# Kernel optimization log

Measured on AMD Instinct MI355X. Metric: run time of the kernel, lower is better.

The kernel has to match this reference:

```python
import jax, jax.numpy as jnp
import numpy as np

D_MODEL = 1024
NHEAD = 16
D_K = D_MODEL // NHEAD


def sparsemax(z):
    # sparsemax along last axis (Martins & Astudillo 2016)
    n = z.shape[-1]
    z_sorted = jnp.flip(jnp.sort(z, axis=-1), axis=-1)          # descending
    k = jnp.arange(1, n + 1, dtype=z.dtype)
    z_cumsum = jnp.cumsum(z_sorted, axis=-1)
    support = (1.0 + k * z_sorted) > z_cumsum                    # [..., n] bool
    k_max = jnp.sum(support, axis=-1, keepdims=True)             # [..., 1] int
    tau_sum = jnp.take_along_axis(z_cumsum, k_max - 1, axis=-1)
    tau = (tau_sum - 1.0) / k_max.astype(z.dtype)
    return jnp.maximum(z - tau, 0.0)


def setup_inputs() -> dict:
    key = jax.random.key(0)
    ks = jax.random.split(key, 12)
    B, S = 2, 2048
    s = 1.0 / np.sqrt(D_MODEL)
    inp = {
        'query': jax.random.normal(ks[0], (B, S, D_MODEL), jnp.float32),
        'key':   jax.random.normal(ks[1], (B, S, D_MODEL), jnp.float32),
        'value': jax.random.normal(ks[2], (B, S, D_MODEL), jnp.float32),
        'Wq': jax.random.uniform(ks[3], (D_MODEL, D_MODEL), jnp.float32, -s, s),
        'bq': jax.random.uniform(ks[4], (D_MODEL,), jnp.float32, -s, s),
        'Wk': jax.random.uniform(ks[5], (D_MODEL, D_MODEL), jnp.float32, -s, s),
        'bk': jax.random.uniform(ks[6], (D_MODEL,), jnp.float32, -s, s),
        'Wv': jax.random.uniform(ks[7], (D_MODEL, D_MODEL), jnp.float32, -s, s),
        'bv': jax.random.uniform(ks[8], (D_MODEL,), jnp.float32, -s, s),
        'Wfc': jax.random.uniform(ks[9], (D_MODEL, D_MODEL), jnp.float32, -s, s),
        'bfc': jax.random.uniform(ks[10], (D_MODEL,), jnp.float32, -s, s),
    }
    return inp


def reference(query, key, value, Wq, bq, Wk, bk, Wv, bv, Wfc, bfc):
    B, S, _ = query.shape
    # projections (torch Linear: x @ W.T + b)
    q = (query @ Wq.T + bq).reshape(B, S, NHEAD, D_K).transpose(0, 2, 1, 3)
    k = (key   @ Wk.T + bk).reshape(B, S, NHEAD, D_K).transpose(0, 2, 1, 3)
    v = (value @ Wv.T + bv).reshape(B, S, NHEAD, D_K).transpose(0, 2, 1, 3)
    # scaled dot-product with sparsemax
    logits = jnp.einsum('bhqd,bhkd->bhqk', q, k) / np.sqrt(D_K).astype(jnp.float32)
    attention = sparsemax(logits)                                # [B,H,S,S]
    attn_out = jnp.einsum('bhqk,bhkd->bhqd', attention, v)
    attn_out = attn_out.transpose(0, 2, 1, 3).reshape(B, S, D_MODEL)
    output = attn_out @ Wfc.T + bfc                              # dropout = identity (eval)
    return output, attention
```

## Files before the change

### kernel.cpp

```cpp
#include <hip/hip_runtime.h>
#include <hip/hip_bf16.h>
#include <cstdint>

#define S_LEN  2048
#define DMODEL 1024
#define NHEAD  16
#define M_ROWS 4096

typedef __attribute__((ext_vector_type(8))) short bf16x8;
typedef __attribute__((ext_vector_type(4))) float f32x4;

__device__ __forceinline__ unsigned short f2bf(float f) {
    __hip_bfloat16 h = __float2bfloat16(f);
    return __builtin_bit_cast(unsigned short, h);
}
__device__ __forceinline__ float bf2f(unsigned short u) {
    return __builtin_bit_cast(float, (unsigned)u << 16);
}
__device__ __forceinline__ uint4 pack8(float4 a, float4 b) {
    uint4 u;
    u.x = ((unsigned)f2bf(a.y) << 16) | f2bf(a.x);
    u.y = ((unsigned)f2bf(a.w) << 16) | f2bf(a.z);
    u.z = ((unsigned)f2bf(b.y) << 16) | f2bf(b.x);
    u.w = ((unsigned)f2bf(b.w) << 16) | f2bf(b.z);
    return u;
}

__device__ __forceinline__ float wave_sum64(float v) {
    v += __shfl_xor(v, 32, 64); v += __shfl_xor(v, 16, 64);
    v += __shfl_xor(v, 8, 64);  v += __shfl_xor(v, 4, 64);
    v += __shfl_xor(v, 2, 64);  v += __shfl_xor(v, 1, 64);
    return v;
}
__device__ __forceinline__ float wave_max64(float v) {
    v = fmaxf(v, __shfl_xor(v, 32, 64)); v = fmaxf(v, __shfl_xor(v, 16, 64));
    v = fmaxf(v, __shfl_xor(v, 8, 64));  v = fmaxf(v, __shfl_xor(v, 4, 64));
    v = fmaxf(v, __shfl_xor(v, 2, 64));  v = fmaxf(v, __shfl_xor(v, 1, 64));
    return v;
}
__device__ __forceinline__ int lanes_below(unsigned long long m) {
    return __builtin_amdgcn_mbcnt_hi((unsigned)(m >> 32),
           __builtin_amdgcn_mbcnt_lo((unsigned)m, 0));
}

__global__ __launch_bounds__(256)
void qkv_gemm(const float* __restrict__ xq, const float* __restrict__ xk,
              const float* __restrict__ xv,
              const float* __restrict__ Wq, const float* __restrict__ Wk,
              const float* __restrict__ Wv,
              const float* __restrict__ bq, const float* __restrict__ bk,
              const float* __restrict__ bv,
              unsigned short* __restrict__ Q_bf, unsigned short* __restrict__ K_bf,
              unsigned short* __restrict__ V_bf) {
    const int which = blockIdx.z;
    const float* A    = (which == 0) ? xq : (which == 1) ? xk : xv;
    const float* W    = (which == 0) ? Wq : (which == 1) ? Wk : Wv;
    const float* bias = (which == 0) ? bq : (which == 1) ? bk : bv;
    unsigned short* dst = (which == 0) ? Q_bf : (which == 1) ? K_bf : V_bf;

    const int row0 = blockIdx.x * 128;
    const int col0 = blockIdx.y * 128;

    __shared__ unsigned short SMEM[10240];
    unsigned short* As = SMEM;
    unsigned short* Bs = SMEM + 5120;

    const int t = threadIdx.x;
    const int wid = t >> 6, lane = t & 63;
    const int wm = wid >> 1, wn = wid & 1;
    const int l = lane & 15, quad = lane >> 4;

    f32x4 acc[4][4];
#pragma unroll
    for (int i = 0; i < 4; ++i)
#pragma unroll
        for (int j = 0; j < 4; ++j) {
            float b_ = bias[col0 + wn * 64 + j * 16 + l];
            acc[i][j] = (f32x4){ b_, b_, b_, b_ };
        }

    for (int k0 = 0; k0 < DMODEL; k0 += 32) {
        uint4 ar[2], br[2];
#pragma unroll
        for (int i = 0; i < 2; ++i) {
            const int c = t + i * 256, r = c >> 2, q = (c & 3) * 8;
            const float* ap = A + (size_t)(row0 + r) * DMODEL + k0 + q;
            const float* wp = W + (size_t)(col0 + r) * DMODEL + k0 + q;
            float4 a0 = *(const float4*)ap, a1 = *(const float4*)(ap + 4);
            float4 w0 = *(const float4*)wp, w1 = *(const float4*)(wp + 4);
            ar[i] = pack8(a0, a1);
            br[i] = pack8(w0, w1);
        }
        __syncthreads();
#pragma unroll
        for (int i = 0; i < 2; ++i) {
            const int c = t + i * 256, r = c >> 2, q = (c & 3) * 8;
            *(uint4*)&As[r * 40 + q] = ar[i];
            *(uint4*)&Bs[r * 40 + q] = br[i];
        }
        __syncthreads();
        bf16x8 a[4], b[4];
#pragma unroll
        for (int i = 0; i < 4; ++i)
            a[i] = *(const bf16x8*)&As[(wm * 64 + i * 16 + l) * 40 + quad * 8];
#pragma unroll
        for (int j = 0; j < 4; ++j)
            b[j] = *(const bf16x8*)&Bs[(wn * 64 + j * 16 + l) * 40 + quad * 8];
#pragma unroll
        for (int i = 0; i < 4; ++i)
#pragma unroll
            for (int j = 0; j < 4; ++j)
                acc[i][j] = __builtin_amdgcn_mfma_f32_16x16x32_bf16(a[i], b[j], acc[i][j], 0, 0, 0);
    }

    __syncthreads();
    unsigned short* Cs = SMEM;
#pragma unroll 1
    for (int jh = 0; jh < 2; ++jh) {
        if (wn == jh) {
#pragma unroll
            for (int i = 0; i < 4; ++i)
#pragma unroll
                for (int j = 0; j < 4; ++j)
#pragma unroll
                    for (int r = 0; r < 4; ++r)
                        Cs[(wm * 64 + i * 16 + quad * 4 + r) * 72 + j * 16 + l] =
                            f2bf(acc[i][j][r]);
        }
        __syncthreads();
#pragma unroll
        for (int it = 0; it < 4; ++it) {
            const int idx = t + it * 256;
            const int row = idx >> 3, c8 = (idx & 7) * 8;
            *(uint4*)(dst + (size_t)(row0 + row) * DMODEL + col0 + jh * 64 + c8) =
                *(const uint4*)&Cs[row * 72 + c8];
        }
        __syncthreads();
    }
}

__global__ __launch_bounds__(256)
void logits_gemm(const unsigned short* __restrict__ Q_bf,
                 const unsigned short* __restrict__ K_bf,
                 float* __restrict__ attn) {
    const int bh = blockIdx.z;
    const int b_ = bh >> 4, h = bh & 15;
    const unsigned short* Qh = Q_bf + ((size_t)b_ * S_LEN) * DMODEL + h * 64;
    const unsigned short* Kh = K_bf + ((size_t)b_ * S_LEN) * DMODEL + h * 64;
    const int row0 = blockIdx.x * 128;
    const int col0 = blockIdx.y * 128;

    __shared__ unsigned short As[128 * 72];
    __shared__ unsigned short Bs[128 * 72];

    const int t = threadIdx.x;
    const int wid = t >> 6, lane = t & 63;
    const int wm = wid >> 1, wn = wid & 1;
    const int l = lane & 15, quad = lane >> 4;

#pragma unroll
    for (int i = 0; i < 4; ++i) {
        const int c = t + i * 256, r = c >> 3, q = (c & 7) * 8;
        *(uint4*)&As[r * 72 + q] = *(const uint4*)(Qh + (size_t)(row0 + r) * DMODEL + q);
        *(uint4*)&Bs[r * 72 + q] = *(const uint4*)(Kh + (size_t)(col0 + r) * DMODEL + q);
    }
    __syncthreads();

    f32x4 acc[4][4] = {};
#pragma unroll
    for (int kk = 0; kk < 64; kk += 32) {
        bf16x8 a[4], b[4];
#pragma unroll
        for (int i = 0; i < 4; ++i)
            a[i] = *(const bf16x8*)&As[(wm * 64 + i * 16 + l) * 72 + kk + quad * 8];
#pragma unroll
        for (int j = 0; j < 4; ++j)
            b[j] = *(const bf16x8*)&Bs[(wn * 64 + j * 16 + l) * 72 + kk + quad * 8];
#pragma unroll
        for (int i = 0; i < 4; ++i)
#pragma unroll
            for (int j = 0; j < 4; ++j)
                acc[i][j] = __builtin_amdgcn_mfma_f32_16x16x32_bf16(a[i], b[j], acc[i][j], 0, 0, 0);
    }

    float* ap = attn + (size_t)bh * S_LEN * S_LEN;
#pragma unroll
    for (int i = 0; i < 4; ++i)
#pragma unroll
        for (int r = 0; r < 4; ++r) {
            const int m = row0 + wm * 64 + i * 16 + quad * 4 + r;
#pragma unroll
            for (int j = 0; j < 4; ++j) {
                const int n = col0 + wn * 64 + j * 16 + l;
                ap[(size_t)m * S_LEN + n] = acc[i][j][r] * 0.125f;
            }
        }
}

__global__ __launch_bounds__(256)
void smpv_kernel(float* __restrict__ attn, const unsigned short* __restrict__ V_bf,
                 unsigned short* __restrict__ AO_bf) {
    const int wave = threadIdx.x >> 6;
    const int lane = threadIdx.x & 63;
    const size_t row = (size_t)blockIdx.x * 4 + wave;
    const int bh = (int)(row >> 11), s = (int)(row & 2047);
    const int b_ = bh >> 4, h = bh & 15;
    float4* rp = (float4*)(attn + row * S_LEN);
    const unsigned short* Vh = V_bf + ((size_t)b_ * S_LEN) * DMODEL + h * 64;

    __shared__ uint2 list[4][512];

    float z[32];
#pragma unroll
    for (int r = 0; r < 8; ++r) {
        float4 v = rp[r * 64 + lane];
        z[4 * r + 0] = v.x; z[4 * r + 1] = v.y;
        z[4 * r + 2] = v.z; z[4 * r + 3] = v.w;
    }
    float m = z[0];
#pragma unroll
    for (int j = 1; j < 32; ++j) m = fmaxf(m, z[j]);
    m = wave_max64(m);

    float tau = m - 1.0f;
#pragma unroll 1
    for (int it = 0; it < 8; ++it) {
        float ss = 0.0f, kk = 0.0f;
#pragma unroll
        for (int j = 0; j < 32; ++j)
            if (z[j] > tau) { ss += z[j]; kk += 1.0f; }
        ss = wave_sum64(ss); kk = wave_sum64(kk);
        tau = (ss - 1.0f) / kk;
    }

#pragma unroll
    for (int j = 0; j < 32; ++j) z[j] = fmaxf(z[j] - tau, 0.0f);
#pragma unroll
    for (int r = 0; r < 8; ++r) {
        float4 v = { z[4 * r + 0], z[4 * r + 1], z[4 * r + 2], z[4 * r + 3] };
        rp[r * 64 + lane] = v;
    }

    float acc = 0.0f;
#pragma unroll 1
    for (int rr = 0; rr < 4; ++rr) {
        int base = 0;
#pragma unroll
        for (int e = 0; e < 8; ++e) {
            const int r = rr * 2 + (e >> 2), jj = e & 3;
            const float pv = z[4 * r + jj];
            const unsigned long long mk = __ballot(pv > 0.0f);
            if (pv > 0.0f) {
                const int pos = base + lanes_below(mk);
                uint2 kp = { (unsigned)(r * 256 + lane * 4 + jj),
                             __builtin_bit_cast(unsigned, pv) };
                list[wave][pos] = kp;
            }
            base += __popcll(mk);
        }
        __threadfence_block();
        const int total = base;
        int i = 0;
        for (; i + 2 <= total; i += 2) {
            uint2 kp0 = list[wave][i], kp1 = list[wave][i + 1];
            float v0 = bf2f(Vh[(size_t)kp0.x * DMODEL + lane]);
            float v1 = bf2f(Vh[(size_t)kp1.x * DMODEL + lane]);
            acc += __builtin_bit_cast(float, kp0.y) * v0;
            acc += __builtin_bit_cast(float, kp1.y) * v1;
        }
        if (i < total) {
            uint2 kp0 = list[wave][i];
            acc += __builtin_bit_cast(float, kp0.y) * bf2f(Vh[(size_t)kp0.x * DMODEL + lane]);
        }
        __threadfence_block();
    }

    AO_bf[((size_t)(b_ * S_LEN + s)) * DMODEL + h * 64 + lane] = f2bf(acc);
}

__global__ __launch_bounds__(256)
void fc_gemm(const unsigned short* __restrict__ AO_bf,
             const float* __restrict__ Wfc,
             const float* __restrict__ bfc, float* __restrict__ out) {
    const int row0 = blockIdx.x * 128;
    const int col0 = blockIdx.y * 128;

    __shared__ unsigned short As[128 * 40];
    __shared__ unsigned short Bs[128 * 40];

    const int t = threadIdx.x;
    const int wid = t >> 6, lane = t & 63;
    const int wm = wid >> 1, wn = wid & 1;
    const int l = lane & 15, quad = lane >> 4;

    f32x4 acc[4][4];
#pragma unroll
    for (int i = 0; i < 4; ++i)
#pragma unroll
        for (int j = 0; j < 4; ++j) {
            float b_ = bfc[col0 + wn * 64 + j * 16 + l];
            acc[i][j] = (f32x4){ b_, b_, b_, b_ };
        }

    for (int k0 = 0; k0 < DMODEL; k0 += 32) {
        uint4 ar[2], br[2];
#pragma unroll
        for (int i = 0; i < 2; ++i) {
            const int c = t + i * 256, r = c >> 2, q = (c & 3) * 8;
            ar[i] = *(const uint4*)(AO_bf + (size_t)(row0 + r) * DMODEL + k0 + q);
            const float* wp = Wfc + (size_t)(col0 + r) * DMODEL + k0 + q;
            float4 w0 = *(const float4*)wp, w1 = *(const float4*)(wp + 4);
            br[i] = pack8(w0, w1);
        }
        __syncthreads();
#pragma unroll
        for (int i = 0; i < 2; ++i) {
            const int c = t + i * 256, r = c >> 2, q = (c & 3) * 8;
            *(uint4*)&As[r * 40 + q] = ar[i];
            *(uint4*)&Bs[r * 40 + q] = br[i];
        }
        __syncthreads();
        bf16x8 a[4], b[4];
#pragma unroll
        for (int i = 0; i < 4; ++i)
            a[i] = *(const bf16x8*)&As[(wm * 64 + i * 16 + l) * 40 + quad * 8];
#pragma unroll
        for (int j = 0; j < 4; ++j)
            b[j] = *(const bf16x8*)&Bs[(wn * 64 + j * 16 + l) * 40 + quad * 8];
#pragma unroll
        for (int i = 0; i < 4; ++i)
#pragma unroll
            for (int j = 0; j < 4; ++j)
                acc[i][j] = __builtin_amdgcn_mfma_f32_16x16x32_bf16(a[i], b[j], acc[i][j], 0, 0, 0);
    }

#pragma unroll
    for (int i = 0; i < 4; ++i)
#pragma unroll
        for (int r = 0; r < 4; ++r) {
            const int m = row0 + wm * 64 + i * 16 + quad * 4 + r;
#pragma unroll
            for (int j = 0; j < 4; ++j) {
                const int n = col0 + wn * 64 + j * 16 + l;
                out[(size_t)m * DMODEL + n] = acc[i][j][r];
            }
        }
}

extern "C" void kernel_launch(void* const* d_in, const int* in_sizes, int n_in,
                              void* d_out, int out_size, void* d_ws, size_t ws_size,
                              hipStream_t stream) {
    const float* q   = (const float*)d_in[0];
    const float* k   = (const float*)d_in[1];
    const float* v   = (const float*)d_in[2];
    const float* Wq  = (const float*)d_in[3];
    const float* bq  = (const float*)d_in[4];
    const float* Wk  = (const float*)d_in[5];
    const float* bk  = (const float*)d_in[6];
    const float* Wv  = (const float*)d_in[7];
    const float* bv  = (const float*)d_in[8];
    const float* Wfc = (const float*)d_in[9];
    const float* bfc = (const float*)d_in[10];

    float* out  = (float*)d_out;
    float* attn = out + (size_t)M_ROWS * DMODEL;

    char* ws = (char*)d_ws;
    unsigned short* Q_bf  = (unsigned short*)ws;
    unsigned short* K_bf  = (unsigned short*)(ws + (8u << 20));
    unsigned short* V_bf  = (unsigned short*)(ws + (16u << 20));
    unsigned short* AO_bf = (unsigned short*)(ws + (24u << 20));

    qkv_gemm<<<dim3(32, 8, 3), 256, 0, stream>>>(q, k, v, Wq, Wk, Wv,
                                                  bq, bk, bv, Q_bf, K_bf, V_bf);
    logits_gemm<<<dim3(16, 16, 32), 256, 0, stream>>>(Q_bf, K_bf, attn);
    smpv_kernel<<<16384, 256, 0, stream>>>(attn, V_bf, AO_bf);
    fc_gemm<<<dim3(32, 8), 256, 0, stream>>>(AO_bf, Wfc, bfc, out);
}
```

Before: 907.4 us.

## Fuse logits, sparsemax and PV into one attention kernel with transposed V

The separate logits GEMM and sparsemax/PV kernels are replaced by one kernel. Each block computes a 16-row strip of scaled logits in registers, finds the sparsemax threshold with cross-wave reductions and writes the attention probabilities once. The PV product then runs on dense bf16 MFMA, reading the probabilities from swizzled LDS and a V tensor that the QKV projection now stores transposed. This removes the write-then-reread of the full attention matrix and the per-row sparse gather over V. In exchange, each block streams its head's K from global memory without LDS staging, and the 64KB LDS buffer limits occupancy.

```diff
diff --git a/kernel.cpp b/kernel.cpp
--- a/kernel.cpp
+++ b/kernel.cpp
@@ -13,9 +13,6 @@
 __device__ __forceinline__ unsigned short f2bf(float f) {
     __hip_bfloat16 h = __float2bfloat16(f);
     return __builtin_bit_cast(unsigned short, h);
-}
-__device__ __forceinline__ float bf2f(unsigned short u) {
-    return __builtin_bit_cast(float, (unsigned)u << 16);
 }
 __device__ __forceinline__ uint4 pack8(float4 a, float4 b) {
     uint4 u;
@@ -24,23 +21,6 @@
     u.z = ((unsigned)f2bf(b.y) << 16) | f2bf(b.x);
     u.w = ((unsigned)f2bf(b.w) << 16) | f2bf(b.z);
     return u;
-}
-
-__device__ __forceinline__ float wave_sum64(float v) {
-    v += __shfl_xor(v, 32, 64); v += __shfl_xor(v, 16, 64);
-    v += __shfl_xor(v, 8, 64);  v += __shfl_xor(v, 4, 64);
-    v += __shfl_xor(v, 2, 64);  v += __shfl_xor(v, 1, 64);
-    return v;
-}
-__device__ __forceinline__ float wave_max64(float v) {
-    v = fmaxf(v, __shfl_xor(v, 32, 64)); v = fmaxf(v, __shfl_xor(v, 16, 64));
-    v = fmaxf(v, __shfl_xor(v, 8, 64));  v = fmaxf(v, __shfl_xor(v, 4, 64));
-    v = fmaxf(v, __shfl_xor(v, 2, 64));  v = fmaxf(v, __shfl_xor(v, 1, 64));
-    return v;
-}
-__device__ __forceinline__ int lanes_below(unsigned long long m) {
-    return __builtin_amdgcn_mbcnt_hi((unsigned)(m >> 32),
-           __builtin_amdgcn_mbcnt_lo((unsigned)m, 0));
 }
 
 __global__ __launch_bounds__(256)
@@ -51,12 +31,12 @@
               const float* __restrict__ bq, const float* __restrict__ bk,
               const float* __restrict__ bv,
               unsigned short* __restrict__ Q_bf, unsigned short* __restrict__ K_bf,
-              unsigned short* __restrict__ V_bf) {
+              unsigned short* __restrict__ V_t) {
     const int which = blockIdx.z;
     const float* A    = (which == 0) ? xq : (which == 1) ? xk : xv;
     const float* W    = (which == 0) ? Wq : (which == 1) ? Wk : Wv;
     const float* bias = (which == 0) ? bq : (which == 1) ? bk : bv;
-    unsigned short* dst = (which == 0) ? Q_bf : (which == 1) ? K_bf : V_bf;
+    unsigned short* dst = (which == 0) ? Q_bf : (which == 1) ? K_bf : V_t;
 
     const int row0 = blockIdx.x * 128;
     const int col0 = blockIdx.y * 128;
@@ -128,154 +108,186 @@
                             f2bf(acc[i][j][r]);
         }
         __syncthreads();
-#pragma unroll
-        for (int it = 0; it < 4; ++it) {
-            const int idx = t + it * 256;
-            const int row = idx >> 3, c8 = (idx & 7) * 8;
-            *(uint4*)(dst + (size_t)(row0 + row) * DMODEL + col0 + jh * 64 + c8) =
-                *(const uint4*)&Cs[row * 72 + c8];
-        }
-        __syncthreads();
-    }
-}
-
-__global__ __launch_bounds__(256)
-void logits_gemm(const unsigned short* __restrict__ Q_bf,
-                 const unsigned short* __restrict__ K_bf,
-                 float* __restrict__ attn) {
-    const int bh = blockIdx.z;
-    const int b_ = bh >> 4, h = bh & 15;
-    const unsigned short* Qh = Q_bf + ((size_t)b_ * S_LEN) * DMODEL + h * 64;
-    const unsigned short* Kh = K_bf + ((size_t)b_ * S_LEN) * DMODEL + h * 64;
-    const int row0 = blockIdx.x * 128;
-    const int col0 = blockIdx.y * 128;
-
-    __shared__ unsigned short As[128 * 72];
-    __shared__ unsigned short Bs[128 * 72];
-
+        if (which == 2) {
+            const int h  = (col0 >> 6) + jh;
+            const int b2 = row0 >> 11;
+            const int s0 = row0 & 2047;
+#pragma unroll
+            for (int it = 0; it < 4; ++it) {
+                const int idx = t + it * 256;
+                const int d = idx & 63, sb = idx >> 6;
+                union { unsigned short u[8]; uint4 v; } tmp;
+#pragma unroll
+                for (int j = 0; j < 8; ++j)
+                    tmp.u[j] = Cs[(sb * 8 + j) * 72 + d];
+                *(uint4*)(dst + ((size_t)((b2 * NHEAD + h) * 64 + d)) * S_LEN
+                                + s0 + sb * 8) = tmp.v;
+            }
+        } else {
+#pragma unroll
+            for (int it = 0; it < 4; ++it) {
+                const int idx = t + it * 256;
+                const int row = idx >> 3, c8 = (idx & 7) * 8;
+                *(uint4*)(dst + (size_t)(row0 + row) * DMODEL + col0 + jh * 64 + c8) =
+                    *(const uint4*)&Cs[row * 72 + c8];
+            }
+        }
+        __syncthreads();
+    }
+}
+
+__global__ __launch_bounds__(512, 4)
+void attn_fused(const unsigned short* __restrict__ Q_bf,
+                const unsigned short* __restrict__ K_bf,
+                const unsigned short* __restrict__ V_t,
+                float* __restrict__ attn,
+                unsigned short* __restrict__ AO_bf) {
     const int t = threadIdx.x;
-    const int wid = t >> 6, lane = t & 63;
-    const int wm = wid >> 1, wn = wid & 1;
+    const int w = t >> 6, lane = t & 63;
     const int l = lane & 15, quad = lane >> 4;
-
-#pragma unroll
-    for (int i = 0; i < 4; ++i) {
-        const int c = t + i * 256, r = c >> 3, q = (c & 7) * 8;
-        *(uint4*)&As[r * 72 + q] = *(const uint4*)(Qh + (size_t)(row0 + r) * DMODEL + q);
-        *(uint4*)&Bs[r * 72 + q] = *(const uint4*)(Kh + (size_t)(col0 + r) * DMODEL + q);
-    }
-    __syncthreads();
-
-    f32x4 acc[4][4] = {};
-#pragma unroll
-    for (int kk = 0; kk < 64; kk += 32) {
-        bf16x8 a[4], b[4];
-#pragma unroll
-        for (int i = 0; i < 4; ++i)
-            a[i] = *(const bf16x8*)&As[(wm * 64 + i * 16 + l) * 72 + kk + quad * 8];
-#pragma unroll
-        for (int j = 0; j < 4; ++j)
-            b[j] = *(const bf16x8*)&Bs[(wn * 64 + j * 16 + l) * 72 + kk + quad * 8];
-#pragma unroll
-        for (int i = 0; i < 4; ++i)
-#pragma unroll
-            for (int j = 0; j < 4; ++j)
-                acc[i][j] = __builtin_amdgcn_mfma_f32_16x16x32_bf16(a[i], b[j], acc[i][j], 0, 0, 0);
-    }
-
-    float* ap = attn + (size_t)bh * S_LEN * S_LEN;
-#pragma unroll
-    for (int i = 0; i < 4; ++i)
-#pragma unroll
-        for (int r = 0; r < 4; ++r) {
-            const int m = row0 + wm * 64 + i * 16 + quad * 4 + r;
-#pragma unroll
-            for (int j = 0; j < 4; ++j) {
-                const int n = col0 + wn * 64 + j * 16 + l;
-                ap[(size_t)m * S_LEN + n] = acc[i][j][r] * 0.125f;
-            }
-        }
-}
-
-__global__ __launch_bounds__(256)
-void smpv_kernel(float* __restrict__ attn, const unsigned short* __restrict__ V_bf,
-                 unsigned short* __restrict__ AO_bf) {
-    const int wave = threadIdx.x >> 6;
-    const int lane = threadIdx.x & 63;
-    const size_t row = (size_t)blockIdx.x * 4 + wave;
-    const int bh = (int)(row >> 11), s = (int)(row & 2047);
-    const int b_ = bh >> 4, h = bh & 15;
-    float4* rp = (float4*)(attn + row * S_LEN);
-    const unsigned short* Vh = V_bf + ((size_t)b_ * S_LEN) * DMODEL + h * 64;
-
-    __shared__ uint2 list[4][512];
-
-    float z[32];
-#pragma unroll
-    for (int r = 0; r < 8; ++r) {
-        float4 v = rp[r * 64 + lane];
-        z[4 * r + 0] = v.x; z[4 * r + 1] = v.y;
-        z[4 * r + 2] = v.z; z[4 * r + 3] = v.w;
-    }
-    float m = z[0];
-#pragma unroll
-    for (int j = 1; j < 32; ++j) m = fmaxf(m, z[j]);
-    m = wave_max64(m);
-
-    float tau = m - 1.0f;
+    const int bh = blockIdx.y, b_ = bh >> 4, h = bh & 15;
+    const int r0 = blockIdx.x * 16;
+
+    __shared__ unsigned short Pl[16 * 2048];
+    __shared__ float redM[8][16];
+    __shared__ float redS[2][8][16];
+    __shared__ float redK[2][8][16];
+    __shared__ float Obuf[4][256];
+
+    const unsigned short* Qp =
+        Q_bf + ((size_t)(b_ * S_LEN + r0 + l)) * DMODEL + h * 64 + quad * 8;
+    const bf16x8 a0 = *(const bf16x8*)Qp;
+    const bf16x8 a1 = *(const bf16x8*)(Qp + 32);
+
+    f32x4 acc[16];
+    const unsigned short* Kb =
+        K_bf + ((size_t)(b_ * S_LEN + w * 256 + l)) * DMODEL + h * 64 + quad * 8;
+#pragma unroll
+    for (int ct = 0; ct < 16; ++ct) {
+        const unsigned short* Kp = Kb + (size_t)(ct * 16) * DMODEL;
+        const bf16x8 b0 = *(const bf16x8*)Kp;
+        const bf16x8 b1 = *(const bf16x8*)(Kp + 32);
+        f32x4 c = {};
+        c = __builtin_amdgcn_mfma_f32_16x16x32_bf16(a0, b0, c, 0, 0, 0);
+        c = __builtin_amdgcn_mfma_f32_16x16x32_bf16(a1, b1, c, 0, 0, 0);
+        acc[ct] = c;
+    }
+#pragma unroll
+    for (int ct = 0; ct < 16; ++ct)
+#pragma unroll
+        for (int r = 0; r < 4; ++r) acc[ct][r] *= 0.125f;
+
+    float tau[4];
+    {
+        float mr[4] = { acc[0][0], acc[0][1], acc[0][2], acc[0][3] };
+#pragma unroll
+        for (int ct = 1; ct < 16; ++ct)
+#pragma unroll
+            for (int r = 0; r < 4; ++r) mr[r] = fmaxf(mr[r], acc[ct][r]);
+#pragma unroll
+        for (int r = 0; r < 4; ++r) {
+            mr[r] = fmaxf(mr[r], __shfl_xor(mr[r], 1, 64));
+            mr[r] = fmaxf(mr[r], __shfl_xor(mr[r], 2, 64));
+            mr[r] = fmaxf(mr[r], __shfl_xor(mr[r], 4, 64));
+            mr[r] = fmaxf(mr[r], __shfl_xor(mr[r], 8, 64));
+        }
+        if (l == 0) {
+#pragma unroll
+            for (int r = 0; r < 4; ++r) redM[w][quad * 4 + r] = mr[r];
+        }
+        __syncthreads();
+#pragma unroll
+        for (int r = 0; r < 4; ++r) {
+            float M = redM[0][quad * 4 + r];
+#pragma unroll
+            for (int w2 = 1; w2 < 8; ++w2) M = fmaxf(M, redM[w2][quad * 4 + r]);
+            tau[r] = M - 1.0f;
+        }
+    }
+
 #pragma unroll 1
     for (int it = 0; it < 8; ++it) {
-        float ss = 0.0f, kk = 0.0f;
-#pragma unroll
-        for (int j = 0; j < 32; ++j)
-            if (z[j] > tau) { ss += z[j]; kk += 1.0f; }
-        ss = wave_sum64(ss); kk = wave_sum64(kk);
-        tau = (ss - 1.0f) / kk;
-    }
-
-#pragma unroll
-    for (int j = 0; j < 32; ++j) z[j] = fmaxf(z[j] - tau, 0.0f);
-#pragma unroll
-    for (int r = 0; r < 8; ++r) {
-        float4 v = { z[4 * r + 0], z[4 * r + 1], z[4 * r + 2], z[4 * r + 3] };
-        rp[r * 64 + lane] = v;
-    }
-
-    float acc = 0.0f;
-#pragma unroll 1
-    for (int rr = 0; rr < 4; ++rr) {
-        int base = 0;
-#pragma unroll
-        for (int e = 0; e < 8; ++e) {
-            const int r = rr * 2 + (e >> 2), jj = e & 3;
-            const float pv = z[4 * r + jj];
-            const unsigned long long mk = __ballot(pv > 0.0f);
-            if (pv > 0.0f) {
-                const int pos = base + lanes_below(mk);
-                uint2 kp = { (unsigned)(r * 256 + lane * 4 + jj),
-                             __builtin_bit_cast(unsigned, pv) };
-                list[wave][pos] = kp;
-            }
-            base += __popcll(mk);
-        }
-        __threadfence_block();
-        const int total = base;
-        int i = 0;
-        for (; i + 2 <= total; i += 2) {
-            uint2 kp0 = list[wave][i], kp1 = list[wave][i + 1];
-            float v0 = bf2f(Vh[(size_t)kp0.x * DMODEL + lane]);
-            float v1 = bf2f(Vh[(size_t)kp1.x * DMODEL + lane]);
-            acc += __builtin_bit_cast(float, kp0.y) * v0;
-            acc += __builtin_bit_cast(float, kp1.y) * v1;
-        }
-        if (i < total) {
-            uint2 kp0 = list[wave][i];
-            acc += __builtin_bit_cast(float, kp0.y) * bf2f(Vh[(size_t)kp0.x * DMODEL + lane]);
-        }
-        __threadfence_block();
-    }
-
-    AO_bf[((size_t)(b_ * S_LEN + s)) * DMODEL + h * 64 + lane] = f2bf(acc);
+        float ss[4] = {}, kk[4] = {};
+#pragma unroll
+        for (int ct = 0; ct < 16; ++ct)
+#pragma unroll
+            for (int r = 0; r < 4; ++r) {
+                const float v = acc[ct][r];
+                if (v > tau[r]) { ss[r] += v; kk[r] += 1.0f; }
+            }
+#pragma unroll
+        for (int r = 0; r < 4; ++r) {
+            ss[r] += __shfl_xor(ss[r], 1, 64); kk[r] += __shfl_xor(kk[r], 1, 64);
+            ss[r] += __shfl_xor(ss[r], 2, 64); kk[r] += __shfl_xor(kk[r], 2, 64);
+            ss[r] += __shfl_xor(ss[r], 4, 64); kk[r] += __shfl_xor(kk[r], 4, 64);
+            ss[r] += __shfl_xor(ss[r], 8, 64); kk[r] += __shfl_xor(kk[r], 8, 64);
+        }
+        const int p = it & 1;
+        if (l == 0) {
+#pragma unroll
+            for (int r = 0; r < 4; ++r) {
+                redS[p][w][quad * 4 + r] = ss[r];
+                redK[p][w][quad * 4 + r] = kk[r];
+            }
+        }
+        __syncthreads();
+#pragma unroll
+        for (int r = 0; r < 4; ++r) {
+            float S = 0.0f, C = 0.0f;
+#pragma unroll
+            for (int w2 = 0; w2 < 8; ++w2) {
+                S += redS[p][w2][quad * 4 + r];
+                C += redK[p][w2][quad * 4 + r];
+            }
+            tau[r] = (S - 1.0f) / C;
+        }
+    }
+
+#pragma unroll
+    for (int ct = 0; ct < 16; ++ct) {
+        const int col = w * 256 + ct * 16 + l;
+#pragma unroll
+        for (int r = 0; r < 4; ++r) {
+            const int row = quad * 4 + r;
+            const float pv = fmaxf(acc[ct][r] - tau[r], 0.0f);
+            acc[ct][r] = pv;
+            Pl[row * 2048 + (col ^ ((row & 7) << 3))] = f2bf(pv);
+        }
+    }
+    __syncthreads();
+
+    float* ap = attn + (size_t)bh * S_LEN * S_LEN;
+#pragma unroll
+    for (int ct = 0; ct < 16; ++ct) {
+        const int col = w * 256 + ct * 16 + l;
+#pragma unroll
+        for (int r = 0; r < 4; ++r)
+            ap[(size_t)(r0 + quad * 4 + r) * S_LEN + col] = acc[ct][r];
+    }
+
+    const int nt = w & 3, kh = w >> 2;
+    f32x4 oacc = {};
+    const unsigned short* Vp =
+        V_t + ((size_t)(bh * 64 + nt * 16 + l)) * S_LEN + kh * 1024 + quad * 8;
+    const int sw = (l & 7) << 3;
+#pragma unroll 4
+    for (int ks = 0; ks < 32; ++ks) {
+        const int k0 = kh * 1024 + ks * 32 + quad * 8;
+        const bf16x8 pa = *(const bf16x8*)&Pl[l * 2048 + (k0 ^ sw)];
+        const bf16x8 vb = *(const bf16x8*)(Vp + ks * 32);
+        oacc = __builtin_amdgcn_mfma_f32_16x16x32_bf16(pa, vb, oacc, 0, 0, 0);
+    }
+    if (kh == 1)
+        *(float4*)&Obuf[nt][lane * 4] = (float4){ oacc[0], oacc[1], oacc[2], oacc[3] };
+    __syncthreads();
+    if (kh == 0) {
+        const float4 o2 = *(const float4*)&Obuf[nt][lane * 4];
+        oacc[0] += o2.x; oacc[1] += o2.y; oacc[2] += o2.z; oacc[3] += o2.w;
+#pragma unroll
+        for (int j = 0; j < 4; ++j)
+            AO_bf[((size_t)(b_ * S_LEN + r0 + quad * 4 + j)) * DMODEL
+                  + h * 64 + nt * 16 + l] = f2bf(oacc[j]);
+    }
 }
 
 __global__ __launch_bounds__(256)
@@ -368,12 +380,11 @@
     char* ws = (char*)d_ws;
     unsigned short* Q_bf  = (unsigned short*)ws;
     unsigned short* K_bf  = (unsigned short*)(ws + (8u << 20));
-    unsigned short* V_bf  = (unsigned short*)(ws + (16u << 20));
+    unsigned short* V_t   = (unsigned short*)(ws + (16u << 20));
     unsigned short* AO_bf = (unsigned short*)(ws + (24u << 20));
 
     qkv_gemm<<<dim3(32, 8, 3), 256, 0, stream>>>(q, k, v, Wq, Wk, Wv,
-                                                  bq, bk, bv, Q_bf, K_bf, V_bf);
-    logits_gemm<<<dim3(16, 16, 32), 256, 0, stream>>>(Q_bf, K_bf, attn);
-    smpv_kernel<<<16384, 256, 0, stream>>>(attn, V_bf, AO_bf);
+                                                  bq, bk, bv, Q_bf, K_bf, V_t);
+    attn_fused<<<dim3(S_LEN / 16, 32), 512, 0, stream>>>(Q_bf, K_bf, V_t, attn, AO_bf);
     fc_gemm<<<dim3(32, 8), 256, 0, stream>>>(AO_bf, Wfc, bfc, out);
 }
```

Result: slower. 1.094 ms (+20.5%).

## Fuse logits GEMM, sparsemax and PV into one attention kernel

Applied to the files above, without the earlier changes.

Merges the logits GEMM and the sparsemax+PV kernel into a single kernel. Each 1024-thread block computes a 16-row logits strip with MFMA, transposes it through LDS into per-wave rows, runs sparsemax and the sparse PV product, and writes the attention matrix once with nontemporal stores. This removes the fp32 logits round trip through HBM (one write plus one read and rewrite). The sparsemax fixed-point loop now exits early once tau stops changing. The trade-off is 64KB of LDS per block, two barrier phases for the transpose, and K tiles read straight from global memory into registers without LDS staging.

```diff
diff --git a/kernel.cpp b/kernel.cpp
--- a/kernel.cpp
+++ b/kernel.cpp
@@ -139,84 +139,61 @@
     }
 }
 
-__global__ __launch_bounds__(256)
-void logits_gemm(const unsigned short* __restrict__ Q_bf,
-                 const unsigned short* __restrict__ K_bf,
-                 float* __restrict__ attn) {
-    const int bh = blockIdx.z;
-    const int b_ = bh >> 4, h = bh & 15;
-    const unsigned short* Qh = Q_bf + ((size_t)b_ * S_LEN) * DMODEL + h * 64;
-    const unsigned short* Kh = K_bf + ((size_t)b_ * S_LEN) * DMODEL + h * 64;
-    const int row0 = blockIdx.x * 128;
-    const int col0 = blockIdx.y * 128;
-
-    __shared__ unsigned short As[128 * 72];
-    __shared__ unsigned short Bs[128 * 72];
-
+__global__ __launch_bounds__(1024, 4)
+void attn_fused(const unsigned short* __restrict__ Q_bf,
+                const unsigned short* __restrict__ K_bf,
+                const unsigned short* __restrict__ V_bf,
+                float* __restrict__ attn,
+                unsigned short* __restrict__ AO_bf) {
     const int t = threadIdx.x;
-    const int wid = t >> 6, lane = t & 63;
-    const int wm = wid >> 1, wn = wid & 1;
+    const int w = t >> 6, lane = t & 63;
     const int l = lane & 15, quad = lane >> 4;
-
-#pragma unroll
-    for (int i = 0; i < 4; ++i) {
-        const int c = t + i * 256, r = c >> 3, q = (c & 7) * 8;
-        *(uint4*)&As[r * 72 + q] = *(const uint4*)(Qh + (size_t)(row0 + r) * DMODEL + q);
-        *(uint4*)&Bs[r * 72 + q] = *(const uint4*)(Kh + (size_t)(col0 + r) * DMODEL + q);
-    }
-    __syncthreads();
-
-    f32x4 acc[4][4] = {};
-#pragma unroll
-    for (int kk = 0; kk < 64; kk += 32) {
-        bf16x8 a[4], b[4];
-#pragma unroll
-        for (int i = 0; i < 4; ++i)
-            a[i] = *(const bf16x8*)&As[(wm * 64 + i * 16 + l) * 72 + kk + quad * 8];
-#pragma unroll
-        for (int j = 0; j < 4; ++j)
-            b[j] = *(const bf16x8*)&Bs[(wn * 64 + j * 16 + l) * 72 + kk + quad * 8];
-#pragma unroll
-        for (int i = 0; i < 4; ++i)
-#pragma unroll
-            for (int j = 0; j < 4; ++j)
-                acc[i][j] = __builtin_amdgcn_mfma_f32_16x16x32_bf16(a[i], b[j], acc[i][j], 0, 0, 0);
-    }
-
-    float* ap = attn + (size_t)bh * S_LEN * S_LEN;
-#pragma unroll
-    for (int i = 0; i < 4; ++i)
-#pragma unroll
-        for (int r = 0; r < 4; ++r) {
-            const int m = row0 + wm * 64 + i * 16 + quad * 4 + r;
-#pragma unroll
-            for (int j = 0; j < 4; ++j) {
-                const int n = col0 + wn * 64 + j * 16 + l;
-                ap[(size_t)m * S_LEN + n] = acc[i][j][r] * 0.125f;
-            }
-        }
-}
-
-__global__ __launch_bounds__(256)
-void smpv_kernel(float* __restrict__ attn, const unsigned short* __restrict__ V_bf,
-                 unsigned short* __restrict__ AO_bf) {
-    const int wave = threadIdx.x >> 6;
-    const int lane = threadIdx.x & 63;
-    const size_t row = (size_t)blockIdx.x * 4 + wave;
-    const int bh = (int)(row >> 11), s = (int)(row & 2047);
-    const int b_ = bh >> 4, h = bh & 15;
-    float4* rp = (float4*)(attn + row * S_LEN);
-    const unsigned short* Vh = V_bf + ((size_t)b_ * S_LEN) * DMODEL + h * 64;
-
-    __shared__ uint2 list[4][512];
+    const int bh = blockIdx.y, b_ = bh >> 4, h = bh & 15;
+    const int r0 = blockIdx.x * 16;
+
+    __shared__ float LDSf[8 * 2048];
+
+    const unsigned short* Qp =
+        Q_bf + ((size_t)(b_ * S_LEN + r0 + l)) * DMODEL + h * 64 + quad * 8;
+    const bf16x8 a0 = *(const bf16x8*)Qp;
+    const bf16x8 a1 = *(const bf16x8*)(Qp + 32);
+
+    f32x4 acc[8];
+    const unsigned short* Kb =
+        K_bf + ((size_t)(b_ * S_LEN + w * 128 + l)) * DMODEL + h * 64 + quad * 8;
+#pragma unroll
+    for (int ct = 0; ct < 8; ++ct) {
+        const unsigned short* Kp = Kb + (size_t)(ct * 16) * DMODEL;
+        const bf16x8 b0 = *(const bf16x8*)Kp;
+        const bf16x8 b1 = *(const bf16x8*)(Kp + 32);
+        f32x4 c = {};
+        c = __builtin_amdgcn_mfma_f32_16x16x32_bf16(a0, b0, c, 0, 0, 0);
+        c = __builtin_amdgcn_mfma_f32_16x16x32_bf16(a1, b1, c, 0, 0, 0);
+#pragma unroll
+        for (int r = 0; r < 4; ++r) c[r] *= 0.125f;
+        acc[ct] = c;
+    }
 
     float z[32];
-#pragma unroll
-    for (int r = 0; r < 8; ++r) {
-        float4 v = rp[r * 64 + lane];
-        z[4 * r + 0] = v.x; z[4 * r + 1] = v.y;
-        z[4 * r + 2] = v.z; z[4 * r + 3] = v.w;
-    }
+#pragma unroll 1
+    for (int c = 0; c < 2; ++c) {
+        if ((quad >> 1) == c) {
+            const int rb = (quad & 1) * 4;
+#pragma unroll
+            for (int ct = 0; ct < 8; ++ct)
+#pragma unroll
+                for (int r = 0; r < 4; ++r)
+                    LDSf[(rb + r) * 2048 + w * 128 + ct * 16 + l] = acc[ct][r];
+        }
+        __syncthreads();
+        if ((w >> 3) == c) {
+#pragma unroll
+            for (int j = 0; j < 32; ++j)
+                z[j] = LDSf[(w & 7) * 2048 + j * 64 + lane];
+        }
+        __syncthreads();
+    }
+
     float m = z[0];
 #pragma unroll
     for (int j = 1; j < 32; ++j) m = fmaxf(m, z[j]);
@@ -230,31 +207,33 @@
         for (int j = 0; j < 32; ++j)
             if (z[j] > tau) { ss += z[j]; kk += 1.0f; }
         ss = wave_sum64(ss); kk = wave_sum64(kk);
-        tau = (ss - 1.0f) / kk;
-    }
-
-#pragma unroll
-    for (int j = 0; j < 32; ++j) z[j] = fmaxf(z[j] - tau, 0.0f);
-#pragma unroll
-    for (int r = 0; r < 8; ++r) {
-        float4 v = { z[4 * r + 0], z[4 * r + 1], z[4 * r + 2], z[4 * r + 3] };
-        rp[r * 64 + lane] = v;
-    }
-
-    float acc = 0.0f;
-#pragma unroll 1
+        const float tn = (ss - 1.0f) / kk;
+        if (tn == tau) break;
+        tau = tn;
+    }
+
+    float* ap = attn + (size_t)bh * S_LEN * S_LEN + (size_t)(r0 + w) * S_LEN;
+#pragma unroll
+    for (int j = 0; j < 32; ++j) {
+        z[j] = fmaxf(z[j] - tau, 0.0f);
+        __builtin_nontemporal_store(z[j], ap + j * 64 + lane);
+    }
+
+    uint2* list = (uint2*)LDSf + w * 512;
+    const unsigned short* Vh = V_bf + ((size_t)b_ * S_LEN) * DMODEL + h * 64;
+    float acco = 0.0f;
+#pragma unroll
     for (int rr = 0; rr < 4; ++rr) {
         int base = 0;
 #pragma unroll
         for (int e = 0; e < 8; ++e) {
-            const int r = rr * 2 + (e >> 2), jj = e & 3;
-            const float pv = z[4 * r + jj];
+            const int j = rr * 8 + e;
+            const float pv = z[j];
             const unsigned long long mk = __ballot(pv > 0.0f);
             if (pv > 0.0f) {
                 const int pos = base + lanes_below(mk);
-                uint2 kp = { (unsigned)(r * 256 + lane * 4 + jj),
-                             __builtin_bit_cast(unsigned, pv) };
-                list[wave][pos] = kp;
+                list[pos] = (uint2){ (unsigned)(j * 64 + lane),
+                                     __builtin_bit_cast(unsigned, pv) };
             }
             base += __popcll(mk);
         }
@@ -262,20 +241,21 @@
         const int total = base;
         int i = 0;
         for (; i + 2 <= total; i += 2) {
-            uint2 kp0 = list[wave][i], kp1 = list[wave][i + 1];
-            float v0 = bf2f(Vh[(size_t)kp0.x * DMODEL + lane]);
-            float v1 = bf2f(Vh[(size_t)kp1.x * DMODEL + lane]);
-            acc += __builtin_bit_cast(float, kp0.y) * v0;
-            acc += __builtin_bit_cast(float, kp1.y) * v1;
+            uint2 k0 = list[i], k1 = list[i + 1];
+            acco += __builtin_bit_cast(float, k0.y) *
+                    bf2f(Vh[(size_t)k0.x * DMODEL + lane]);
+            acco += __builtin_bit_cast(float, k1.y) *
+                    bf2f(Vh[(size_t)k1.x * DMODEL + lane]);
         }
         if (i < total) {
-            uint2 kp0 = list[wave][i];
-            acc += __builtin_bit_cast(float, kp0.y) * bf2f(Vh[(size_t)kp0.x * DMODEL + lane]);
+            uint2 k0 = list[i];
+            acco += __builtin_bit_cast(float, k0.y) *
+                    bf2f(Vh[(size_t)k0.x * DMODEL + lane]);
         }
         __threadfence_block();
     }
 
-    AO_bf[((size_t)(b_ * S_LEN + s)) * DMODEL + h * 64 + lane] = f2bf(acc);
+    AO_bf[((size_t)(b_ * S_LEN + r0 + w)) * DMODEL + h * 64 + lane] = f2bf(acco);
 }
 
 __global__ __launch_bounds__(256)
@@ -373,7 +353,6 @@
 
     qkv_gemm<<<dim3(32, 8, 3), 256, 0, stream>>>(q, k, v, Wq, Wk, Wv,
                                                   bq, bk, bv, Q_bf, K_bf, V_bf);
-    logits_gemm<<<dim3(16, 16, 32), 256, 0, stream>>>(Q_bf, K_bf, attn);
-    smpv_kernel<<<16384, 256, 0, stream>>>(attn, V_bf, AO_bf);
+    attn_fused<<<dim3(S_LEN / 16, 32), 1024, 0, stream>>>(Q_bf, K_bf, V_bf, attn, AO_bf);
     fc_gemm<<<dim3(32, 8), 256, 0, stream>>>(AO_bf, Wfc, bfc, out);
 }
```

Result: slower. 934.5 us (+3.0%).
